# Kernel optimization log

Measured on AMD Instinct MI355X. Metric: run time of the kernel, lower is better.

Reference implementation:

```python
import jax, jax.numpy as jnp
import numpy as np
import math

DIM = 1024
H = 16
HD = DIM // H  # 64
M = 64         # num_features
B, S = 4, 4096


def setup_inputs() -> dict:
    key = jax.random.key(0)
    ks = jax.random.split(key, 10)
    sc = 1.0 / math.sqrt(DIM)
    return {
        "x": jax.random.normal(ks[0], (B, S, DIM), dtype=jnp.float32),
        "Wq": jax.random.normal(ks[1], (DIM, DIM), dtype=jnp.float32) * sc,
        "bq": jax.random.normal(ks[2], (DIM,), dtype=jnp.float32) * 0.01,
        "Wk": jax.random.normal(ks[3], (DIM, DIM), dtype=jnp.float32) * sc,
        "bk": jax.random.normal(ks[4], (DIM,), dtype=jnp.float32) * 0.01,
        "Wv": jax.random.normal(ks[5], (DIM, DIM), dtype=jnp.float32) * sc,
        "bv": jax.random.normal(ks[6], (DIM,), dtype=jnp.float32) * 0.01,
        "Wo": jax.random.normal(ks[7], (DIM, DIM), dtype=jnp.float32) * sc,
        "bo": jax.random.normal(ks[8], (DIM,), dtype=jnp.float32) * 0.01,
        "P": jax.random.normal(ks[9], (H, M, HD), dtype=jnp.float32),
    }


def _feature_map(t, P):
    # t: [b,h,s,d], P: [h,m,d] -> relu(t @ P^T) / sqrt(m)
    proj = jnp.einsum("bhsd,hmd->bhsm", t, P)
    return jax.nn.relu(proj) * (1.0 / math.sqrt(P.shape[1]))


def reference(x, Wq, bq, Wk, bk, Wv, bv, Wo, bo, P):
    b, s, dim = x.shape
    h, m, hd = P.shape
    # Linear projections (torch Linear: x @ W^T + b), split heads -> [b,h,s,hd]
    def split_heads(y):
        return y.reshape(b, s, h, hd).transpose(0, 2, 1, 3)
    q = split_heads(x @ Wq.T + bq)
    k = split_heads(x @ Wk.T + bk)
    v = split_heads(x @ Wv.T + bv)
    q_prime = _feature_map(q, P)  # [b,h,s,m]
    k_prime = _feature_map(k, P)  # [b,h,s,m]
    kv = jnp.einsum("bhsm,bhsd->bhmd", k_prime, v)       # [b,h,m,hd]
    attn = jnp.einsum("bhsm,bhmd->bhsd", q_prime, kv)    # [b,h,s,hd]
    attn = attn.transpose(0, 2, 1, 3).reshape(b, s, dim)
    return attn @ Wo.T + bo
```

## Files before the change

### kernel.cpp

```cpp
#include <hip/hip_runtime.h>
#include <hip/hip_bf16.h>
#include <cstdint>

typedef __bf16 bf16_t;
typedef bf16_t bf16x8 __attribute__((ext_vector_type(8)));
typedef float f32x4 __attribute__((ext_vector_type(4)));


__device__ __forceinline__ void gload_lds16(const bf16_t* g, bf16_t* l) {
  __builtin_amdgcn_global_load_lds(
      (const __attribute__((address_space(1))) uint32_t*)g,
      (__attribute__((address_space(3))) uint32_t*)l, 16, 0, 0);
}

__global__ void cast_f32_bf16(const float* __restrict__ in, bf16_t* __restrict__ out, int n8) {
  int i = blockIdx.x * 256 + threadIdx.x;
  if (i < n8) {
    const f32x4* p = (const f32x4*)(in + (long)i * 8);
    f32x4 a = p[0], b = p[1];
    bf16x8 o;
#pragma unroll
    for (int j = 0; j < 4; ++j) { o[j] = (bf16_t)a[j]; o[j + 4] = (bf16_t)b[j]; }
    *(bf16x8*)(out + (long)i * 8) = o;
  }
}

__global__ void copy_f32(const float* __restrict__ in, float* __restrict__ out, int n) {
  int i = blockIdx.x * 256 + threadIdx.x;
  if (i < n) out[i] = in[i];
}

__global__ __launch_bounds__(256) void prep_wqk(
    const float* __restrict__ Wq, const float* __restrict__ bq,
    const float* __restrict__ Wk, const float* __restrict__ bk,
    const float* __restrict__ P,
    bf16_t* __restrict__ Wcat, float* __restrict__ bcat)
{
  int bid = blockIdx.x;
  int qk = bid >> 7, h = (bid >> 3) & 15, kt = bid & 7;
  const float* W = qk ? Wk : Wq;
  const float* bias = qk ? bk : bq;
  __shared__ float Pl[64 * 64];
  __shared__ float Wlt[128 * 68];
  int t = threadIdx.x;
  int k0 = kt * 128;
  for (int i = t * 4; i < 4096; i += 1024)
    *(f32x4*)&Pl[i] = *(const f32x4*)&P[h * 4096 + i];
  for (int fi = t; fi < 2048; fi += 256) {
    int row = fi >> 5;
    int c4 = fi & 31;
    f32x4 w = *(const f32x4*)&W[(long)(h * 64 + row) * 1024 + k0 + c4 * 4];
#pragma unroll
    for (int j = 0; j < 4; ++j) Wlt[(c4 * 4 + j) * 68 + row] = w[j];
  }
  __syncthreads();
  int kloc = t >> 1;
  int mh = (t & 1) * 32;
  for (int m = mh; m < mh + 32; ++m) {
    f32x4 s = {0.f, 0.f, 0.f, 0.f};
#pragma unroll
    for (int dd = 0; dd < 16; ++dd)
      s += (*(const f32x4*)&Pl[m * 64 + dd * 4]) * (*(const f32x4*)&Wlt[kloc * 68 + dd * 4]);
    float a = s[0] + s[1] + s[2] + s[3];
    Wcat[(long)(qk * 1024 + h * 64 + m) * 1024 + k0 + kloc] = (bf16_t)a;
  }
  if (kt == 0 && t < 64) {
    float a = 0.f;
    for (int d = 0; d < 64; ++d) a += Pl[t * 64 + d] * bias[h * 64 + d];
    bcat[qk * 1024 + h * 64 + t] = a;
  }
}

template <int EPI>
__global__ __launch_bounds__(512, 2) void gemm256(
    const bf16_t* __restrict__ A, int lda,
    const bf16_t* __restrict__ B0, int ldb,
    const float* __restrict__ bias,
    void* __restrict__ Cv, int ldc,
    int K, int ncols, int cpx,
    int rows_per_batch, long bstride)
{
  __shared__ bf16_t sA[2][16384];
  __shared__ bf16_t sB[2][16384];

  const int lin = blockIdx.x;
  const int wgid = (lin & 7) * cpx + (lin >> 3);
  const int row0 = (wgid / ncols) * 256;
  const int col0 = (wgid % ncols) * 256;

  const int tid = threadIdx.x;
  const int w = tid >> 6, l = tid & 63;
  const int wr = w >> 2, wc = w & 3;
  const int llo = l & 15, lhi = l >> 4;
  const int x7 = llo & 7;

  const bf16_t* Bm = B0 + (long)(row0 / rows_per_batch) * bstride;

  long a_off[4], b_off[4];
#pragma unroll
  for (int i = 0; i < 4; ++i) {
    int c = i * 512 + tid;
    int r = c >> 3;
    int kqs = (c & 7) ^ (r & 7);
    a_off[i] = (long)(row0 + r) * lda + kqs * 8;
    b_off[i] = (long)(col0 + r) * ldb + kqs * 8;
  }
  const int ldst = tid * 8;

  const int aoff0 = ((lhi)     ^ x7) * 8;
  const int aoff1 = ((lhi + 4) ^ x7) * 8;
  const int abase = (wr * 128 + llo) * 64;
  const int bbase = (wc * 64 + llo) * 64;

  f32x4 acc[8][4] = {};
  const int NT = K >> 6;

#pragma unroll
  for (int i = 0; i < 4; ++i) {
    gload_lds16(A + a_off[i], &sA[0][i * 4096 + ldst]);
    gload_lds16(Bm + b_off[i], &sB[0][i * 4096 + ldst]);
  }
  __syncthreads();

#define TILE_BODY(PC, PN, T)                                                            \
  {                                                                                     \
    bf16x8 bfr[4][2], afr[4][2];                                                        \
    _Pragma("unroll") for (int ni = 0; ni < 4; ++ni) {                                  \
      bfr[ni][0] = *(const bf16x8*)&sB[PC][bbase + ni * 1024 + aoff0];                  \
      bfr[ni][1] = *(const bf16x8*)&sB[PC][bbase + ni * 1024 + aoff1];                  \
    }                                                                                   \
    _Pragma("unroll") for (int mi = 0; mi < 4; ++mi) {                                  \
      afr[mi][0] = *(const bf16x8*)&sA[PC][abase + mi * 1024 + aoff0];                  \
      afr[mi][1] = *(const bf16x8*)&sA[PC][abase + mi * 1024 + aoff1];                  \
    }                                                                                   \
    if ((T) + 1 < NT) {                                                                 \
      long ks = (long)((T) + 1) * 64;                                                   \
      _Pragma("unroll") for (int i = 0; i < 4; ++i) {                                   \
        gload_lds16(A + a_off[i] + ks, &sA[PN][i * 4096 + ldst]);                       \
        gload_lds16(Bm + b_off[i] + ks, &sB[PN][i * 4096 + ldst]);                      \
      }                                                                                 \
    }                                                                                   \
    __builtin_amdgcn_s_setprio(1);                                                      \
    _Pragma("unroll") for (int mi = 0; mi < 4; ++mi)                                    \
      _Pragma("unroll") for (int ni = 0; ni < 4; ++ni) {                                \
        acc[mi][ni] = __builtin_amdgcn_mfma_f32_16x16x32_bf16(afr[mi][0], bfr[ni][0], acc[mi][ni], 0, 0, 0); \
        acc[mi][ni] = __builtin_amdgcn_mfma_f32_16x16x32_bf16(afr[mi][1], bfr[ni][1], acc[mi][ni], 0, 0, 0); \
      }                                                                                 \
    __builtin_amdgcn_s_setprio(0);                                                      \
    _Pragma("unroll") for (int mi = 0; mi < 4; ++mi) {                                  \
      afr[mi][0] = *(const bf16x8*)&sA[PC][abase + (mi + 4) * 1024 + aoff0];            \
      afr[mi][1] = *(const bf16x8*)&sA[PC][abase + (mi + 4) * 1024 + aoff1];            \
    }                                                                                   \
    __builtin_amdgcn_s_setprio(1);                                                      \
    _Pragma("unroll") for (int mi = 0; mi < 4; ++mi)                                    \
      _Pragma("unroll") for (int ni = 0; ni < 4; ++ni) {                                \
        acc[mi + 4][ni] = __builtin_amdgcn_mfma_f32_16x16x32_bf16(afr[mi][0], bfr[ni][0], acc[mi + 4][ni], 0, 0, 0); \
        acc[mi + 4][ni] = __builtin_amdgcn_mfma_f32_16x16x32_bf16(afr[mi][1], bfr[ni][1], acc[mi + 4][ni], 0, 0, 0); \
      }                                                                                 \
    __builtin_amdgcn_s_setprio(0);                                                      \
    __syncthreads();                                                                    \
  }

  for (int t = 0; t < NT; t += 2) {
    TILE_BODY(0, 1, t);
    TILE_BODY(1, 0, t + 1);
  }
#undef TILE_BODY

#pragma unroll
  for (int ni = 0; ni < 4; ++ni) {
    const int gcol = col0 + wc * 64 + ni * 16 + llo;
    const float bz = bias[gcol];
#pragma unroll
    for (int mi = 0; mi < 8; ++mi) {
      const int grow0 = row0 + wr * 128 + mi * 16 + lhi * 4;
#pragma unroll
      for (int j = 0; j < 4; ++j) {
        float v = acc[mi][ni][j] + bz;
        if constexpr (EPI == 1) { if (gcol < 2048) v = fmaxf(v, 0.f) * 0.125f; }
        if constexpr (EPI == 2)
          ((float*)Cv)[(long)(grow0 + j) * ldc + gcol] = v;
        else
          ((bf16_t*)Cv)[(long)(grow0 + j) * ldc + gcol] = (bf16_t)v;
      }
    }
  }
}

__global__ __launch_bounds__(256) void kv_partial(
    const bf16_t* __restrict__ QKV, float* __restrict__ kvpart)
{
  int bh = blockIdx.x;
  int split = blockIdx.y;
  int b = bh >> 4, h = bh & 15;
  __shared__ alignas(16) bf16_t Kt[64 * 32];
  __shared__ alignas(16) bf16_t Vt[64 * 32];
  int t = threadIdx.x;
  int wv = t >> 6, lane = t & 63, lhi = lane >> 4, llo = lane & 15;
  int r = t >> 3;
  int c = (t & 7) * 8;
  f32x4 acc[4] = {};
  long rowbase = ((long)b * 4096 + split * 512) * 3072 + h * 64 + c;
  for (int sc = 0; sc < 16; ++sc) {
    long off = rowbase + (long)(sc * 32 + r) * 3072;
    bf16x8 kk = *(const bf16x8*)(QKV + off + 1024);
    bf16x8 vvv = *(const bf16x8*)(QKV + off + 2048);
#pragma unroll
    for (int j = 0; j < 8; ++j) {
      Kt[(c + j) * 32 + r] = kk[j];
      Vt[(c + j) * 32 + r] = vvv[j];
    }
    __syncthreads();
    bf16x8 a = *(const bf16x8*)&Kt[(wv * 16 + llo) * 32 + lhi * 8];
#pragma unroll
    for (int ni = 0; ni < 4; ++ni) {
      bf16x8 bb = *(const bf16x8*)&Vt[(ni * 16 + llo) * 32 + lhi * 8];
      acc[ni] = __builtin_amdgcn_mfma_f32_16x16x32_bf16(a, bb, acc[ni], 0, 0, 0);
    }
    __syncthreads();
  }
#pragma unroll
  for (int ni = 0; ni < 4; ++ni)
#pragma unroll
    for (int j = 0; j < 4; ++j) {
      int m = wv * 16 + lhi * 4 + j;
      int d = ni * 16 + llo;
      kvpart[((long)split * 64 + bh) * 4096 + m * 64 + d] = acc[ni][j];
    }
}

__global__ void kv_reduce(const float* __restrict__ part, float* __restrict__ kv) {
  int i = blockIdx.x * 256 + threadIdx.x;
  float s = 0.f;
#pragma unroll
  for (int sp = 0; sp < 8; ++sp) s += part[sp * 262144 + i];
  kv[i] = s;
}

__global__ __launch_bounds__(256) void wcombt_kernel(
    const float* __restrict__ kv, const float* __restrict__ Wo,
    bf16_t* __restrict__ WcT)
{
  int nt = blockIdx.x, h = blockIdx.y, b = blockIdx.z;
  __shared__ float kvs[4096];
  int t = threadIdx.x;
  for (int i = t * 4; i < 4096; i += 1024)
    *(f32x4*)&kvs[i] = *(const f32x4*)&kv[((long)b * 16 + h) * 4096 + i];
  __syncthreads();
  int n = nt * 128 + (t >> 1);
  int mh = (t & 1) * 32;
  f32x4 wo[16];
#pragma unroll
  for (int dd = 0; dd < 16; ++dd) wo[dd] = *(const f32x4*)&Wo[(long)n * 1024 + h * 64 + dd * 4];
  for (int m = mh; m < mh + 32; ++m) {
    f32x4 s = {0.f, 0.f, 0.f, 0.f};
#pragma unroll
    for (int dd = 0; dd < 16; ++dd)
      s += (*(const f32x4*)&kvs[m * 64 + dd * 4]) * wo[dd];
    WcT[((long)b * 1024 + n) * 1024 + h * 64 + m] = (bf16_t)(s[0] + s[1] + s[2] + s[3]);
  }
}

extern "C" void kernel_launch(void* const* d_in, const int* in_sizes, int n_in,
                              void* d_out, int out_size, void* d_ws, size_t ws_size,
                              hipStream_t stream) {
  (void)in_sizes; (void)n_in; (void)out_size; (void)ws_size;
  const float* x  = (const float*)d_in[0];
  const float* Wq = (const float*)d_in[1];
  const float* bq = (const float*)d_in[2];
  const float* Wk = (const float*)d_in[3];
  const float* bk = (const float*)d_in[4];
  const float* Wv = (const float*)d_in[5];
  const float* bv = (const float*)d_in[6];
  const float* Wo = (const float*)d_in[7];
  const float* bo = (const float*)d_in[8];
  const float* P  = (const float*)d_in[9];
  float* out = (float*)d_out;

  char* ws = (char*)d_ws;
  bf16_t* xb     = (bf16_t*)(ws + 0);
  bf16_t* QKV    = (bf16_t*)(ws + 33554432);
  bf16_t* Wcat   = (bf16_t*)(ws + 134217728);
  float*  bcat   = (float*) (ws + 140509184);
  float*  kvpart = (float*) (ws + 140521472);
  float*  kvbuf  = (float*) (ws + 148910080);
  bf16_t* WcT    = (bf16_t*)(ws + 149958656);

  cast_f32_bf16<<<8192, 256, 0, stream>>>(x, xb, 2097152);
  cast_f32_bf16<<<512, 256, 0, stream>>>(Wv, Wcat + (size_t)2048 * 1024, 131072);
  copy_f32<<<4, 256, 0, stream>>>(bv, bcat + 2048, 1024);
  prep_wqk<<<256, 256, 0, stream>>>(Wq, bq, Wk, bk, P, Wcat, bcat);

  gemm256<1><<<768, 512, 0, stream>>>(
      xb, 1024, Wcat, 1024, bcat, QKV, 3072, 1024, 12, 96, 1 << 30, 0);

  kv_partial<<<dim3(64, 8), 256, 0, stream>>>(QKV, kvpart);
  kv_reduce<<<1024, 256, 0, stream>>>(kvpart, kvbuf);

  wcombt_kernel<<<dim3(8, 16, 4), 256, 0, stream>>>(kvbuf, Wo, WcT);

  gemm256<2><<<256, 512, 0, stream>>>(
      QKV, 3072, WcT, 1024, bo, out, 1024, 1024, 4, 32, 4096, (long)1024 * 1024);
}
```

Baseline: 236.9 us.

## Split GEMM k-tile into four quarter stages with fine-grained vmcnt barriers

Rewrites the GEMM main loop so each 64-wide k-tile is processed in four quarters. Each quarter waits only on its own slice of the previous async LDS loads (s_waitcnt vmcnt plus s_barrier), then issues the matching slice of next-tile loads and runs its MFMAs. This replaces the single full __syncthreads per tile. The row mapping of warps is also interleaved (wr*32 within 64-row groups) so every quarter of the A tile feeds all warps, and the epilogue row index changes to match. The aim is to overlap global-to-LDS traffic with MFMA more finely, at the cost of more barriers and correctness that depends on the exact ordering of the vmcnt counts.

```diff
diff --git a/kernel.cpp b/kernel.cpp
--- a/kernel.cpp
+++ b/kernel.cpp
@@ -71,6 +71,57 @@
   }
 }
 
+#define WB(N) asm volatile("s_waitcnt vmcnt(" #N ")\n\ts_barrier" ::: "memory")
+
+#define MFMA16(J, A00, A01, A10, A11)                                                   \
+    __builtin_amdgcn_s_setprio(1);                                                     \
+    _Pragma("unroll") for (int ni = 0; ni < 4; ++ni) {                                  \
+      acc[2*(J)][ni]   = __builtin_amdgcn_mfma_f32_16x16x32_bf16(A00, bfr[ni][0], acc[2*(J)][ni], 0, 0, 0);   \
+      acc[2*(J)][ni]   = __builtin_amdgcn_mfma_f32_16x16x32_bf16(A01, bfr[ni][1], acc[2*(J)][ni], 0, 0, 0);   \
+      acc[2*(J)+1][ni] = __builtin_amdgcn_mfma_f32_16x16x32_bf16(A10, bfr[ni][0], acc[2*(J)+1][ni], 0, 0, 0); \
+      acc[2*(J)+1][ni] = __builtin_amdgcn_mfma_f32_16x16x32_bf16(A11, bfr[ni][1], acc[2*(J)+1][ni], 0, 0, 0); \
+    }                                                                                   \
+    __builtin_amdgcn_s_setprio(0);
+
+#define TILE(sAc, sBc, sAn, sBn, KN, STG, W0, W1, W2, W3) {                             \
+  WB(W0);                                                                               \
+  _Pragma("unroll") for (int ni = 0; ni < 4; ++ni) {                                    \
+    bfr[ni][0] = *(const bf16x8*)&sBc[wc4096 + ni * 1024 + base0];                      \
+    bfr[ni][1] = *(const bf16x8*)&sBc[wc4096 + ni * 1024 + base1];                      \
+  }                                                                                     \
+  { bf16x8 a00 = *(const bf16x8*)&sAc[wr2048 + base0];                                  \
+    bf16x8 a01 = *(const bf16x8*)&sAc[wr2048 + base1];                                  \
+    bf16x8 a10 = *(const bf16x8*)&sAc[wr2048 + 1024 + base0];                           \
+    bf16x8 a11 = *(const bf16x8*)&sAc[wr2048 + 1024 + base1];                           \
+    if (STG) { gload_lds16(Bm + b_off[0] + (KN), &sBn[dst8]);                           \
+               gload_lds16(Bm + b_off[1] + (KN), &sBn[4096 + dst8]); }                  \
+    MFMA16(0, a00, a01, a10, a11) }                                                     \
+  WB(W1);                                                                               \
+  { bf16x8 a00 = *(const bf16x8*)&sAc[4096 + wr2048 + base0];                           \
+    bf16x8 a01 = *(const bf16x8*)&sAc[4096 + wr2048 + base1];                           \
+    bf16x8 a10 = *(const bf16x8*)&sAc[4096 + wr2048 + 1024 + base0];                    \
+    bf16x8 a11 = *(const bf16x8*)&sAc[4096 + wr2048 + 1024 + base1];                    \
+    if (STG) { gload_lds16(Bm + b_off[2] + (KN), &sBn[8192 + dst8]);                    \
+               gload_lds16(Bm + b_off[3] + (KN), &sBn[12288 + dst8]); }                 \
+    MFMA16(1, a00, a01, a10, a11) }                                                     \
+  WB(W2);                                                                               \
+  { bf16x8 a00 = *(const bf16x8*)&sAc[8192 + wr2048 + base0];                           \
+    bf16x8 a01 = *(const bf16x8*)&sAc[8192 + wr2048 + base1];                           \
+    bf16x8 a10 = *(const bf16x8*)&sAc[8192 + wr2048 + 1024 + base0];                    \
+    bf16x8 a11 = *(const bf16x8*)&sAc[8192 + wr2048 + 1024 + base1];                    \
+    if (STG) { gload_lds16(A + a_off[0] + (KN), &sAn[dst8]);                            \
+               gload_lds16(A + a_off[1] + (KN), &sAn[4096 + dst8]); }                   \
+    MFMA16(2, a00, a01, a10, a11) }                                                     \
+  WB(W3);                                                                               \
+  { bf16x8 a00 = *(const bf16x8*)&sAc[12288 + wr2048 + base0];                          \
+    bf16x8 a01 = *(const bf16x8*)&sAc[12288 + wr2048 + base1];                          \
+    bf16x8 a10 = *(const bf16x8*)&sAc[12288 + wr2048 + 1024 + base0];                   \
+    bf16x8 a11 = *(const bf16x8*)&sAc[12288 + wr2048 + 1024 + base1];                   \
+    if (STG) { gload_lds16(A + a_off[2] + (KN), &sAn[8192 + dst8]);                     \
+               gload_lds16(A + a_off[3] + (KN), &sAn[12288 + dst8]); }                  \
+    MFMA16(3, a00, a01, a10, a11) }                                                     \
+}
+
 template <int EPI>
 __global__ __launch_bounds__(512, 2) void gemm256(
     const bf16_t* __restrict__ A, int lda,
@@ -80,8 +131,8 @@
     int K, int ncols, int cpx,
     int rows_per_batch, long bstride)
 {
-  __shared__ bf16_t sA[2][16384];
-  __shared__ bf16_t sB[2][16384];
+  __shared__ alignas(16) bf16_t sA0[16384], sA1[16384];
+  __shared__ alignas(16) bf16_t sB0[16384], sB1[16384];
 
   const int lin = blockIdx.x;
   const int wgid = (lin & 7) * cpx + (lin >> 3);
@@ -105,67 +156,33 @@
     a_off[i] = (long)(row0 + r) * lda + kqs * 8;
     b_off[i] = (long)(col0 + r) * ldb + kqs * 8;
   }
-  const int ldst = tid * 8;
-
-  const int aoff0 = ((lhi)     ^ x7) * 8;
-  const int aoff1 = ((lhi + 4) ^ x7) * 8;
-  const int abase = (wr * 128 + llo) * 64;
-  const int bbase = (wc * 64 + llo) * 64;
+  const int dst8 = tid * 8;
+
+  const int base0 = llo * 64 + ((lhi)     ^ x7) * 8;
+  const int base1 = llo * 64 + ((lhi + 4) ^ x7) * 8;
+  const int wr2048 = wr * 2048;
+  const int wc4096 = wc * 4096;
 
   f32x4 acc[8][4] = {};
+  bf16x8 bfr[4][2];
   const int NT = K >> 6;
 
-#pragma unroll
-  for (int i = 0; i < 4; ++i) {
-    gload_lds16(A + a_off[i], &sA[0][i * 4096 + ldst]);
-    gload_lds16(Bm + b_off[i], &sB[0][i * 4096 + ldst]);
-  }
-  __syncthreads();
-
-#define TILE_BODY(PC, PN, T)                                                            \
-  {                                                                                     \
-    bf16x8 bfr[4][2], afr[4][2];                                                        \
-    _Pragma("unroll") for (int ni = 0; ni < 4; ++ni) {                                  \
-      bfr[ni][0] = *(const bf16x8*)&sB[PC][bbase + ni * 1024 + aoff0];                  \
-      bfr[ni][1] = *(const bf16x8*)&sB[PC][bbase + ni * 1024 + aoff1];                  \
-    }                                                                                   \
-    _Pragma("unroll") for (int mi = 0; mi < 4; ++mi) {                                  \
-      afr[mi][0] = *(const bf16x8*)&sA[PC][abase + mi * 1024 + aoff0];                  \
-      afr[mi][1] = *(const bf16x8*)&sA[PC][abase + mi * 1024 + aoff1];                  \
-    }                                                                                   \
-    if ((T) + 1 < NT) {                                                                 \
-      long ks = (long)((T) + 1) * 64;                                                   \
-      _Pragma("unroll") for (int i = 0; i < 4; ++i) {                                   \
-        gload_lds16(A + a_off[i] + ks, &sA[PN][i * 4096 + ldst]);                       \
-        gload_lds16(Bm + b_off[i] + ks, &sB[PN][i * 4096 + ldst]);                      \
-      }                                                                                 \
-    }                                                                                   \
-    __builtin_amdgcn_s_setprio(1);                                                      \
-    _Pragma("unroll") for (int mi = 0; mi < 4; ++mi)                                    \
-      _Pragma("unroll") for (int ni = 0; ni < 4; ++ni) {                                \
-        acc[mi][ni] = __builtin_amdgcn_mfma_f32_16x16x32_bf16(afr[mi][0], bfr[ni][0], acc[mi][ni], 0, 0, 0); \
-        acc[mi][ni] = __builtin_amdgcn_mfma_f32_16x16x32_bf16(afr[mi][1], bfr[ni][1], acc[mi][ni], 0, 0, 0); \
-      }                                                                                 \
-    __builtin_amdgcn_s_setprio(0);                                                      \
-    _Pragma("unroll") for (int mi = 0; mi < 4; ++mi) {                                  \
-      afr[mi][0] = *(const bf16x8*)&sA[PC][abase + (mi + 4) * 1024 + aoff0];            \
-      afr[mi][1] = *(const bf16x8*)&sA[PC][abase + (mi + 4) * 1024 + aoff1];            \
-    }                                                                                   \
-    __builtin_amdgcn_s_setprio(1);                                                      \
-    _Pragma("unroll") for (int mi = 0; mi < 4; ++mi)                                    \
-      _Pragma("unroll") for (int ni = 0; ni < 4; ++ni) {                                \
-        acc[mi + 4][ni] = __builtin_amdgcn_mfma_f32_16x16x32_bf16(afr[mi][0], bfr[ni][0], acc[mi + 4][ni], 0, 0, 0); \
-        acc[mi + 4][ni] = __builtin_amdgcn_mfma_f32_16x16x32_bf16(afr[mi][1], bfr[ni][1], acc[mi + 4][ni], 0, 0, 0); \
-      }                                                                                 \
-    __builtin_amdgcn_s_setprio(0);                                                      \
-    __syncthreads();                                                                    \
-  }
-
-  for (int t = 0; t < NT; t += 2) {
-    TILE_BODY(0, 1, t);
-    TILE_BODY(1, 0, t + 1);
-  }
-#undef TILE_BODY
+  gload_lds16(Bm + b_off[0], &sB0[dst8]);
+  gload_lds16(Bm + b_off[1], &sB0[4096 + dst8]);
+  gload_lds16(Bm + b_off[2], &sB0[8192 + dst8]);
+  gload_lds16(Bm + b_off[3], &sB0[12288 + dst8]);
+  gload_lds16(A + a_off[0], &sA0[dst8]);
+  gload_lds16(A + a_off[1], &sA0[4096 + dst8]);
+  gload_lds16(A + a_off[2], &sA0[8192 + dst8]);
+  gload_lds16(A + a_off[3], &sA0[12288 + dst8]);
+
+  int t = 0;
+  for (; t < NT - 2; t += 2) {
+    TILE(sA0, sB0, sA1, sB1, (long)(t + 1) * 64, 1, 3, 4, 5, 6);
+    TILE(sA1, sB1, sA0, sB0, (long)(t + 2) * 64, 1, 3, 4, 5, 6);
+  }
+  TILE(sA0, sB0, sA1, sB1, (long)(NT - 1) * 64, 1, 3, 4, 5, 6);
+  TILE(sA1, sB1, sA0, sB0, 0L, 0, 3, 2, 1, 0);
 
 #pragma unroll
   for (int ni = 0; ni < 4; ++ni) {
@@ -173,7 +190,7 @@
     const float bz = bias[gcol];
 #pragma unroll
     for (int mi = 0; mi < 8; ++mi) {
-      const int grow0 = row0 + wr * 128 + mi * 16 + lhi * 4;
+      const int grow0 = row0 + (mi >> 1) * 64 + wr * 32 + (mi & 1) * 16 + lhi * 4;
 #pragma unroll
       for (int j = 0; j < 4; ++j) {
         float v = acc[mi][ni][j] + bz;
```

Result: slower. 254.6 us (+7.5%).

## Restructure GEMM main loop into four-phase pipeline with split-K LDS staging

Applied to the files above, without the earlier changes.

Replaces the two-tile double-buffered GEMM loop with a four-phase schedule. Each 64-wide K tile is split into two 32-wide halves in a new LDS layout, so global-to-LDS loads for the next tile are issued in quarters between MFMA blocks. Fragment loads for the next phase are prefetched into registers while the current MFMAs run. Explicit vmcnt waits and raw s_barrier replace __syncthreads so loads overlap compute more finely. The cost is more complex synchronisation, higher register pressure from four fragment buffers, and a risk of races if the waitcnt counts are wrong.

```diff
diff --git a/kernel.cpp b/kernel.cpp
--- a/kernel.cpp
+++ b/kernel.cpp
@@ -71,6 +71,56 @@
   }
 }
 
+#define VMW(N) asm volatile("s_waitcnt vmcnt(" #N ")" ::: "memory")
+#define SBAR() __builtin_amdgcn_s_barrier()
+
+#define AFRAG(dst, P, KH, MIB)                                                      \
+  _Pragma("unroll") for (int i = 0; i < 4; ++i)                                     \
+    dst[i] = *(const bf16x8*)&smem[(P)*16384 + (KH)*8192 + ((MIB)+i)*1024 + llo64 + aoffA];
+
+#define BFRAG(dst, P, KH)                                                           \
+  _Pragma("unroll") for (int n = 0; n < 4; ++n)                                     \
+    dst[n] = *(const bf16x8*)&smem[32768 + (P)*16384 + (KH)*8192 + bbase + n*1024 + boffB];
+
+#define STAGE_A(P, KH, KOFF) {                                                      \
+  gload_lds16(A + a_off0 + (KOFF) + (KH)*32, &smem[(P)*16384 + (KH)*8192 + dst8]);  \
+  gload_lds16(A + a_off1 + (KOFF) + (KH)*32, &smem[(P)*16384 + (KH)*8192 + 4096 + dst8]); }
+
+#define STAGE_B(P, KH, KOFF) {                                                      \
+  gload_lds16(Bm + b_off0 + (KOFF) + (KH)*32, &smem[32768 + (P)*16384 + (KH)*8192 + dst8]); \
+  gload_lds16(Bm + b_off1 + (KOFF) + (KH)*32, &smem[32768 + (P)*16384 + (KH)*8192 + 4096 + dst8]); }
+
+#define MFMA_BLK(MIB, AF, BF)                                                       \
+  __builtin_amdgcn_s_setprio(1);                                                    \
+  _Pragma("unroll") for (int mi = 0; mi < 4; ++mi)                                  \
+    _Pragma("unroll") for (int ni = 0; ni < 4; ++ni)                                \
+      acc[(MIB)+mi][ni] = __builtin_amdgcn_mfma_f32_16x16x32_bf16(AF[mi], BF[ni], acc[(MIB)+mi][ni], 0, 0, 0); \
+  __builtin_amdgcn_s_setprio(0);
+
+#define PH1(P, Q, KOFF, STG, WN) {                                                  \
+  AFRAG(afr1, P, 0, 4);                                                             \
+  if (STG) STAGE_A(Q, 0, KOFF);                                                     \
+  MFMA_BLK(0, afr0, bfr0);                                                          \
+  VMW(WN); SBAR(); }
+
+#define PH2(P, Q, KOFF, STG) {                                                      \
+  BFRAG(bfr1, P, 1); AFRAG(afr0, P, 1, 0);                                          \
+  if (STG) STAGE_B(Q, 0, KOFF);                                                     \
+  MFMA_BLK(4, afr1, bfr0);                                                          \
+  SBAR(); }
+
+#define PH3(P, Q, KOFF, STG, WN) {                                                  \
+  AFRAG(afr1, P, 1, 4);                                                             \
+  if (STG) STAGE_A(Q, 1, KOFF);                                                     \
+  MFMA_BLK(0, afr0, bfr1);                                                          \
+  VMW(WN); SBAR(); }
+
+#define PH4(P, Q, KOFF, STG, LAST) {                                                \
+  if (!(LAST)) { BFRAG(bfr0, Q, 0); AFRAG(afr0, Q, 0, 0); }                         \
+  if (STG) STAGE_B(Q, 1, KOFF);                                                     \
+  MFMA_BLK(4, afr1, bfr1);                                                          \
+  if (!(LAST)) SBAR(); }
+
 template <int EPI>
 __global__ __launch_bounds__(512, 2) void gemm256(
     const bf16_t* __restrict__ A, int lda,
@@ -80,8 +130,7 @@
     int K, int ncols, int cpx,
     int rows_per_batch, long bstride)
 {
-  __shared__ bf16_t sA[2][16384];
-  __shared__ bf16_t sB[2][16384];
+  __shared__ alignas(16) bf16_t smem[65536];
 
   const int lin = blockIdx.x;
   const int wgid = (lin & 7) * cpx + (lin >> 3);
@@ -96,76 +145,47 @@
 
   const bf16_t* Bm = B0 + (long)(row0 / rows_per_batch) * bstride;
 
-  long a_off[4], b_off[4];
-#pragma unroll
-  for (int i = 0; i < 4; ++i) {
-    int c = i * 512 + tid;
-    int r = c >> 3;
-    int kqs = (c & 7) ^ (r & 7);
-    a_off[i] = (long)(row0 + r) * lda + kqs * 8;
-    b_off[i] = (long)(col0 + r) * ldb + kqs * 8;
-  }
-  const int ldst = tid * 8;
-
-  const int aoff0 = ((lhi)     ^ x7) * 8;
-  const int aoff1 = ((lhi + 4) ^ x7) * 8;
-  const int abase = (wr * 128 + llo) * 64;
-  const int bbase = (wc * 64 + llo) * 64;
+  long a_off0, a_off1, b_off0, b_off1;
+  {
+    int c0 = tid, c1 = 512 + tid;
+    int r0 = c0 >> 3, cc0 = (c0 & 7) ^ (r0 & 7);
+    int r1 = c1 >> 3, cc1 = (c1 & 7) ^ (r1 & 7);
+    int srow0 = r0 + ((cc0 >> 2) << 7), skq0 = cc0 & 3;
+    int srow1 = r1 + ((cc1 >> 2) << 7), skq1 = cc1 & 3;
+    a_off0 = (long)(row0 + srow0) * lda + skq0 * 8;
+    a_off1 = (long)(row0 + srow1) * lda + skq1 * 8;
+    b_off0 = (long)(col0 + srow0) * ldb + skq0 * 8;
+    b_off1 = (long)(col0 + srow1) * ldb + skq1 * 8;
+  }
+  const int dst8 = tid * 8;
+
+  const int llo64 = llo * 64;
+  const int aoffA = ((lhi + 4 * wr) ^ x7) * 8;
+  const int bbase = (wc & 1) * 4096 + llo * 64;
+  const int boffB = ((lhi + 4 * (wc >> 1)) ^ x7) * 8;
 
   f32x4 acc[8][4] = {};
+  bf16x8 afr0[4], afr1[4], bfr0[4], bfr1[4];
   const int NT = K >> 6;
 
-#pragma unroll
-  for (int i = 0; i < 4; ++i) {
-    gload_lds16(A + a_off[i], &sA[0][i * 4096 + ldst]);
-    gload_lds16(Bm + b_off[i], &sB[0][i * 4096 + ldst]);
-  }
-  __syncthreads();
-
-#define TILE_BODY(PC, PN, T)                                                            \
-  {                                                                                     \
-    bf16x8 bfr[4][2], afr[4][2];                                                        \
-    _Pragma("unroll") for (int ni = 0; ni < 4; ++ni) {                                  \
-      bfr[ni][0] = *(const bf16x8*)&sB[PC][bbase + ni * 1024 + aoff0];                  \
-      bfr[ni][1] = *(const bf16x8*)&sB[PC][bbase + ni * 1024 + aoff1];                  \
-    }                                                                                   \
-    _Pragma("unroll") for (int mi = 0; mi < 4; ++mi) {                                  \
-      afr[mi][0] = *(const bf16x8*)&sA[PC][abase + mi * 1024 + aoff0];                  \
-      afr[mi][1] = *(const bf16x8*)&sA[PC][abase + mi * 1024 + aoff1];                  \
-    }                                                                                   \
-    if ((T) + 1 < NT) {                                                                 \
-      long ks = (long)((T) + 1) * 64;                                                   \
-      _Pragma("unroll") for (int i = 0; i < 4; ++i) {                                   \
-        gload_lds16(A + a_off[i] + ks, &sA[PN][i * 4096 + ldst]);                       \
-        gload_lds16(Bm + b_off[i] + ks, &sB[PN][i * 4096 + ldst]);                      \
-      }                                                                                 \
-    }                                                                                   \
-    __builtin_amdgcn_s_setprio(1);                                                      \
-    _Pragma("unroll") for (int mi = 0; mi < 4; ++mi)                                    \
-      _Pragma("unroll") for (int ni = 0; ni < 4; ++ni) {                                \
-        acc[mi][ni] = __builtin_amdgcn_mfma_f32_16x16x32_bf16(afr[mi][0], bfr[ni][0], acc[mi][ni], 0, 0, 0); \
-        acc[mi][ni] = __builtin_amdgcn_mfma_f32_16x16x32_bf16(afr[mi][1], bfr[ni][1], acc[mi][ni], 0, 0, 0); \
-      }                                                                                 \
-    __builtin_amdgcn_s_setprio(0);                                                      \
-    _Pragma("unroll") for (int mi = 0; mi < 4; ++mi) {                                  \
-      afr[mi][0] = *(const bf16x8*)&sA[PC][abase + (mi + 4) * 1024 + aoff0];            \
-      afr[mi][1] = *(const bf16x8*)&sA[PC][abase + (mi + 4) * 1024 + aoff1];            \
-    }                                                                                   \
-    __builtin_amdgcn_s_setprio(1);                                                      \
-    _Pragma("unroll") for (int mi = 0; mi < 4; ++mi)                                    \
-      _Pragma("unroll") for (int ni = 0; ni < 4; ++ni) {                                \
-        acc[mi + 4][ni] = __builtin_amdgcn_mfma_f32_16x16x32_bf16(afr[mi][0], bfr[ni][0], acc[mi + 4][ni], 0, 0, 0); \
-        acc[mi + 4][ni] = __builtin_amdgcn_mfma_f32_16x16x32_bf16(afr[mi][1], bfr[ni][1], acc[mi + 4][ni], 0, 0, 0); \
-      }                                                                                 \
-    __builtin_amdgcn_s_setprio(0);                                                      \
-    __syncthreads();                                                                    \
-  }
-
-  for (int t = 0; t < NT; t += 2) {
-    TILE_BODY(0, 1, t);
-    TILE_BODY(1, 0, t + 1);
-  }
-#undef TILE_BODY
+  STAGE_A(0, 0, 0L); STAGE_B(0, 0, 0L);
+  STAGE_A(0, 1, 0L); STAGE_B(0, 1, 0L);
+  VMW(4); SBAR();
+  BFRAG(bfr0, 0, 0); AFRAG(afr0, 0, 0, 0);
+
+  int t = 0;
+  for (; t < NT - 2; t += 2) {
+    const long k1 = (long)(t + 1) * 64, k2 = (long)(t + 2) * 64;
+    PH1(0, 1, k1, 1, 2); PH2(0, 1, k1, 1); PH3(0, 1, k1, 1, 2); PH4(0, 1, k1, 1, 0);
+    PH1(1, 0, k2, 1, 2); PH2(1, 0, k2, 1); PH3(1, 0, k2, 1, 2); PH4(1, 0, k2, 1, 0);
+  }
+  {
+    const long kL = (long)(NT - 1) * 64;
+    PH1(0, 1, kL, 1, 2); PH2(0, 1, kL, 1); PH3(0, 1, kL, 1, 2); PH4(0, 1, kL, 1, 0);
+  }
+  {
+    PH1(1, 0, 0L, 0, 0); PH2(1, 0, 0L, 0); PH3(1, 0, 0L, 0, 0); PH4(1, 0, 0L, 0, 1);
+  }
 
 #pragma unroll
   for (int ni = 0; ni < 4; ++ni) {
```

Result: slower. 243.8 us (+2.9%).

## Merge prep cast kernels and use 128x128 tile GEMM for output projection

Applied to the files above, without the earlier changes.

Combines the x cast, the Wv cast and the bv copy into a single launch so that two kernel launches go away. The final output GEMM (16384x1024x1024) changes from a 256x256-tile kernel running 256 workgroups to a new 128x128-tile kernel running 1024 workgroups with launch_bounds(512,4). The aim is to fill more of the CUs, since 256 workgroups leaves the MI355X partly idle. In exchange, each workgroup reuses less data per tile and generates more global and LDS traffic.

```diff
diff --git a/kernel.cpp b/kernel.cpp
--- a/kernel.cpp
+++ b/kernel.cpp
@@ -13,21 +13,30 @@
       (__attribute__((address_space(3))) uint32_t*)l, 16, 0, 0);
 }
 
-__global__ void cast_f32_bf16(const float* __restrict__ in, bf16_t* __restrict__ out, int n8) {
-  int i = blockIdx.x * 256 + threadIdx.x;
-  if (i < n8) {
-    const f32x4* p = (const f32x4*)(in + (long)i * 8);
-    f32x4 a = p[0], b = p[1];
+__global__ void prep_misc(const float* __restrict__ x, const float* __restrict__ Wv,
+                          const float* __restrict__ bv,
+                          bf16_t* __restrict__ xb, bf16_t* __restrict__ WvO,
+                          float* __restrict__ bcat) {
+  int b = blockIdx.x, t = threadIdx.x;
+  if (b < 8192) {
+    long i = (long)b * 256 + t;
+    const f32x4* p = (const f32x4*)(x + i * 8);
+    f32x4 a = p[0], c = p[1];
     bf16x8 o;
 #pragma unroll
-    for (int j = 0; j < 4; ++j) { o[j] = (bf16_t)a[j]; o[j + 4] = (bf16_t)b[j]; }
-    *(bf16x8*)(out + (long)i * 8) = o;
-  }
-}
-
-__global__ void copy_f32(const float* __restrict__ in, float* __restrict__ out, int n) {
-  int i = blockIdx.x * 256 + threadIdx.x;
-  if (i < n) out[i] = in[i];
+    for (int j = 0; j < 4; ++j) { o[j] = (bf16_t)a[j]; o[j + 4] = (bf16_t)c[j]; }
+    *(bf16x8*)(xb + i * 8) = o;
+  } else if (b < 8704) {
+    long i = (long)(b - 8192) * 256 + t;
+    const f32x4* p = (const f32x4*)(Wv + i * 8);
+    f32x4 a = p[0], c = p[1];
+    bf16x8 o;
+#pragma unroll
+    for (int j = 0; j < 4; ++j) { o[j] = (bf16_t)a[j]; o[j + 4] = (bf16_t)c[j]; }
+    *(bf16x8*)(WvO + i * 8) = o;
+  } else {
+    *(f32x4*)&bcat[2048 + t * 4] = *(const f32x4*)&bv[t * 4];
+  }
 }
 
 __global__ __launch_bounds__(256) void prep_wqk(
@@ -187,6 +196,104 @@
   }
 }
 
+__global__ __launch_bounds__(512, 4) void gemm128(
+    const bf16_t* __restrict__ A, int lda,
+    const bf16_t* __restrict__ B0, int ldb,
+    const float* __restrict__ bias,
+    float* __restrict__ C, int ldc,
+    int K, int ncols, int cpx,
+    int rows_per_batch, long bstride)
+{
+  __shared__ bf16_t sA[2][8192];
+  __shared__ bf16_t sB[2][8192];
+
+  const int lin = blockIdx.x;
+  const int wgid = (lin & 7) * cpx + (lin >> 3);
+  const int row0 = (wgid / ncols) * 128;
+  const int col0 = (wgid % ncols) * 128;
+
+  const int tid = threadIdx.x;
+  const int w = tid >> 6, l = tid & 63;
+  const int wr = w >> 2, wc = w & 3;
+  const int llo = l & 15, lhi = l >> 4;
+  const int x7 = llo & 7;
+
+  const bf16_t* Bm = B0 + (long)(row0 / rows_per_batch) * bstride;
+
+  long a_off[2], b_off[2];
+#pragma unroll
+  for (int i = 0; i < 2; ++i) {
+    int c = i * 512 + tid;
+    int r = c >> 3;
+    int kqs = (c & 7) ^ (r & 7);
+    a_off[i] = (long)(row0 + r) * lda + kqs * 8;
+    b_off[i] = (long)(col0 + r) * ldb + kqs * 8;
+  }
+  const int ldst = tid * 8;
+
+  const int aoff0 = ((lhi)     ^ x7) * 8;
+  const int aoff1 = ((lhi + 4) ^ x7) * 8;
+  const int abase = (wr * 64 + llo) * 64;
+  const int bbase = (wc * 32 + llo) * 64;
+
+  f32x4 acc[4][2] = {};
+  const int NT = K >> 6;
+
+#pragma unroll
+  for (int i = 0; i < 2; ++i) {
+    gload_lds16(A + a_off[i], &sA[0][i * 4096 + ldst]);
+    gload_lds16(Bm + b_off[i], &sB[0][i * 4096 + ldst]);
+  }
+  __syncthreads();
+
+#define TILE128(PC, PN, T)                                                              \
+  {                                                                                     \
+    bf16x8 bfr[2][2], afr[4][2];                                                        \
+    _Pragma("unroll") for (int ni = 0; ni < 2; ++ni) {                                  \
+      bfr[ni][0] = *(const bf16x8*)&sB[PC][bbase + ni * 1024 + aoff0];                  \
+      bfr[ni][1] = *(const bf16x8*)&sB[PC][bbase + ni * 1024 + aoff1];                  \
+    }                                                                                   \
+    _Pragma("unroll") for (int mi = 0; mi < 4; ++mi) {                                  \
+      afr[mi][0] = *(const bf16x8*)&sA[PC][abase + mi * 1024 + aoff0];                  \
+      afr[mi][1] = *(const bf16x8*)&sA[PC][abase + mi * 1024 + aoff1];                  \
+    }                                                                                   \
+    if ((T) + 1 < NT) {                                                                 \
+      long ks = (long)((T) + 1) * 64;                                                   \
+      _Pragma("unroll") for (int i = 0; i < 2; ++i) {                                   \
+        gload_lds16(A + a_off[i] + ks, &sA[PN][i * 4096 + ldst]);                       \
+        gload_lds16(Bm + b_off[i] + ks, &sB[PN][i * 4096 + ldst]);                      \
+      }                                                                                 \
+    }                                                                                   \
+    __builtin_amdgcn_s_setprio(1);                                                      \
+    _Pragma("unroll") for (int mi = 0; mi < 4; ++mi)                                    \
+      _Pragma("unroll") for (int ni = 0; ni < 2; ++ni) {                                \
+        acc[mi][ni] = __builtin_amdgcn_mfma_f32_16x16x32_bf16(afr[mi][0], bfr[ni][0], acc[mi][ni], 0, 0, 0); \
+        acc[mi][ni] = __builtin_amdgcn_mfma_f32_16x16x32_bf16(afr[mi][1], bfr[ni][1], acc[mi][ni], 0, 0, 0); \
+      }                                                                                 \
+    __builtin_amdgcn_s_setprio(0);                                                      \
+    __syncthreads();                                                                    \
+  }
+
+  for (int t = 0; t < NT; t += 2) {
+    TILE128(0, 1, t);
+    TILE128(1, 0, t + 1);
+  }
+#undef TILE128
+
+#pragma unroll
+  for (int ni = 0; ni < 2; ++ni) {
+    const int gcol = col0 + wc * 32 + ni * 16 + llo;
+    const float bz = bias[gcol];
+#pragma unroll
+    for (int mi = 0; mi < 4; ++mi) {
+      const int grow0 = row0 + wr * 64 + mi * 16 + lhi * 4;
+#pragma unroll
+      for (int j = 0; j < 4; ++j)
+        C[(long)(grow0 + j) * ldc + gcol] = acc[mi][ni][j] + bz;
+    }
+  }
+}
+
 __global__ __launch_bounds__(256) void kv_partial(
     const bf16_t* __restrict__ QKV, float* __restrict__ kvpart)
 {
@@ -286,9 +393,7 @@
   float*  kvbuf  = (float*) (ws + 148910080);
   bf16_t* WcT    = (bf16_t*)(ws + 149958656);
 
-  cast_f32_bf16<<<8192, 256, 0, stream>>>(x, xb, 2097152);
-  cast_f32_bf16<<<512, 256, 0, stream>>>(Wv, Wcat + (size_t)2048 * 1024, 131072);
-  copy_f32<<<4, 256, 0, stream>>>(bv, bcat + 2048, 1024);
+  prep_misc<<<8705, 256, 0, stream>>>(x, Wv, bv, xb, Wcat + (size_t)2048 * 1024, bcat);
   prep_wqk<<<256, 256, 0, stream>>>(Wq, bq, Wk, bk, P, Wcat, bcat);
 
   gemm256<1><<<768, 512, 0, stream>>>(
@@ -299,6 +404,6 @@
 
   wcombt_kernel<<<dim3(8, 16, 4), 256, 0, stream>>>(kvbuf, Wo, WcT);
 
-  gemm256<2><<<256, 512, 0, stream>>>(
-      QKV, 3072, WcT, 1024, bo, out, 1024, 1024, 4, 32, 4096, (long)1024 * 1024);
-}
+  gemm128<<<1024, 512, 0, stream>>>(
+      QKV, 3072, WcT, 1024, bo, out, 1024, 1024, 8, 128, 4096, (long)1024 * 1024);
+}
```

After: 233.8 us. About the same (-1.3%).
